# Optimization experiments

Measured on AMD Instinct MI355X. Metric: run time of the kernel, lower is better.

The kernel has to match this reference:

```python
import jax, jax.numpy as jnp
import numpy as np

N, S, D = 8, 448, 768
VS, DS = 50000, 256
VP, DP = 200, 128
VM, DM = 400, 128
VA, DA = 360, 128
EPS_LS = 0.1
LN_EPS = 1e-12
SQRT2 = 1.4142135623730951


def setup_inputs() -> dict:
    key = jax.random.key(0)
    ks = jax.random.split(key, 20)
    total = N * S
    # all sequence lengths == S; next-token prediction uses tokens [0, S-2] as
    # inputs (hidden_sel) and tokens [1, S-1] as targets (target_sel)
    hidden_sel = np.concatenate([i * S + np.arange(S - 1) for i in range(N)]).astype(np.int32)
    target_sel = np.concatenate([i * S + np.arange(1, S) for i in range(N)]).astype(np.int32)
    tokens_lengths = (np.arange(total) % 4).astype(np.int32)  # per-token affix counts
    affix_sel = np.nonzero(tokens_lengths[target_sel] > 0)[0].astype(np.int32)

    def p(k, shape):
        return jax.random.normal(k, shape, jnp.float32) * 0.02

    inp = {
        "tr_hidden_state": jax.random.normal(ks[0], (S, N, D), jnp.float32),
        "affixes_prob": jax.random.uniform(ks[1], (total, VA), dtype=jnp.float32),
        "stems": jax.random.randint(ks[2], (total,), 0, VS, jnp.int32),
        "pos_tags": jax.random.randint(ks[3], (total,), 0, VP, jnp.int32),
        "lm_morphs": jax.random.randint(ks[4], (total,), 0, VM, jnp.int32),
        "hidden_sel_idx": jnp.asarray(hidden_sel),
        "target_sel_idx": jnp.asarray(target_sel),
        "affix_sel_idx": jnp.asarray(affix_sel),
        # stem head
        "stem_emb": p(ks[5], (VS, DS)), "stem_W": p(ks[6], (D, DS)),
        "stem_b": jnp.zeros((DS,)), "stem_g": jnp.ones((DS,)),
        "stem_beta": jnp.zeros((DS,)), "stem_bias": jnp.zeros((VS,)),
        # pos-tag head
        "pos_emb": p(ks[7], (VP, DP)), "pos_W": p(ks[8], (D, DP)),
        "pos_b": jnp.zeros((DP,)), "pos_g": jnp.ones((DP,)),
        "pos_beta": jnp.zeros((DP,)), "pos_bias": jnp.zeros((VP,)),
        # lm-morph head
        "morph_emb": p(ks[9], (VM, DM)), "morph_W": p(ks[10], (D, DM)),
        "morph_b": jnp.zeros((DM,)), "morph_g": jnp.ones((DM,)),
        "morph_beta": jnp.zeros((DM,)), "morph_bias": jnp.zeros((VM,)),
        # affixes head
        "aff_emb": p(ks[11], (VA, DA)), "aff_W": p(ks[12], (D, DA)),
        "aff_b": jnp.zeros((DA,)), "aff_g": jnp.ones((DA,)),
        "aff_beta": jnp.zeros((DA,)), "aff_bias": jnp.zeros((VA,)),
    }
    return inp


def _gelu(x):
    return x * 0.5 * (1.0 + jax.lax.erf(x / SQRT2))


def _ln(x, g, b):
    m = x.mean(-1, keepdims=True)
    v = ((x - m) ** 2).mean(-1, keepdims=True)
    return (x - m) * jax.lax.rsqrt(v + LN_EPS) * g + b


def _head(x, W, b, g, beta, emb, bias):
    h = _ln(_gelu(x @ W + b), g, beta)  # BaseHeadTransform
    return h @ emb.T + bias             # tied decoder + bias


def _ls_nll(lprobs, tgt):
    # label_smoothed_nll_loss with reduce=True, no ignore_index
    nll = -jnp.take_along_axis(lprobs, tgt[:, None], axis=1)[:, 0]
    smooth = -lprobs.sum(-1)
    nll_m, sm_m = nll.mean(), smooth.mean()
    eps_i = EPS_LS / (lprobs.shape[-1] - 1)
    return (1.0 - EPS_LS - eps_i) * nll_m + eps_i * sm_m, nll_m


def reference(tr_hidden_state, affixes_prob, stems, pos_tags, lm_morphs,
              hidden_sel_idx, target_sel_idx, affix_sel_idx,
              stem_emb, stem_W, stem_b, stem_g, stem_beta, stem_bias,
              pos_emb, pos_W, pos_b, pos_g, pos_beta, pos_bias,
              morph_emb, morph_W, morph_b, morph_g, morph_beta, morph_bias,
              aff_emb, aff_W, aff_b, aff_g, aff_beta, aff_bias):
    flat = jnp.transpose(tr_hidden_state, (1, 0, 2)).reshape(N * S, D)
    x = flat[hidden_sel_idx]  # [T, D] ragged gather of predictor states

    stem_lp = jax.nn.log_softmax(_head(x, stem_W, stem_b, stem_g, stem_beta, stem_emb, stem_bias), axis=-1)
    stem_loss, stem_nll = _ls_nll(stem_lp, stems[target_sel_idx])

    pos_lp = jax.nn.log_softmax(_head(x, pos_W, pos_b, pos_g, pos_beta, pos_emb, pos_bias), axis=-1)
    pos_loss, pos_nll = _ls_nll(pos_lp, pos_tags[target_sel_idx])

    morph_lp = jax.nn.log_softmax(_head(x, morph_W, morph_b, morph_g, morph_beta, morph_emb, morph_bias), axis=-1)
    morph_loss, morph_nll = _ls_nll(morph_lp, lm_morphs[target_sel_idx])

    xa = x[affix_sel_idx]                                # tokens with affixes
    ta = affixes_prob[target_sel_idx][affix_sel_idx]     # [Ta, VA]
    z = _head(xa, aff_W, aff_b, aff_g, aff_beta, aff_emb, aff_bias)
    aff_loss = jnp.mean(jnp.maximum(z, 0.0) - z * ta + jnp.log1p(jnp.exp(-jnp.abs(z))))

    return jnp.stack([stem_loss, pos_loss, morph_loss, aff_loss, stem_nll, pos_nll, morph_nll])
```

## Files before the change

kernel.cpp:

```cpp
#include <hip/hip_runtime.h>
#include <cstdint>
#include <cstddef>


typedef __attribute__((ext_vector_type(8))) __bf16 bf16x8;
typedef __attribute__((ext_vector_type(4))) float f32x4;
typedef __attribute__((ext_vector_type(4))) unsigned short u16x4;
typedef __attribute__((ext_vector_type(2))) unsigned short u16x2;

namespace {
constexpr int S_LEN   = 448;
constexpr int N_SEQ   = 8;
constexpr int D_MODEL = 768;
constexpr int TPAD    = 3584;
constexpr int VS = 50000, VP = 200, VM = 400, VA = 360;
constexpr int DS_STEM = 256, DS_POS = 128, DS_MORPH = 128, DS_AFF = 128;
constexpr int VS_PAD = 50176;
constexpr int VCHUNK = 32;
constexpr int VITERS = 3136 / VCHUNK;
constexpr int PERIODS = VITERS / 2;
constexpr float PAD_E = (float)(VS_PAD - VS);
constexpr int NVB_P = 1;
constexpr int NVB_M = 2;
constexpr float LOG2E = 1.4426950408889634f;
constexpr float LN2   = 0.6931471805599453f;
constexpr int B_STEM = 448;
constexpr int B_P    = B_STEM + 112;
constexpr int B_M    = B_P + 224;
constexpr int PREP_G = TPAD * D_MODEL / 256;
constexpr int PREP_T = PREP_G + 491520 / 256;
constexpr int PREP_C = PREP_T + 12753;
}

__device__ __forceinline__ unsigned short f2bf(float f) {
  unsigned int u = __float_as_uint(f);
  unsigned int r = (u + 0x7FFFu + ((u >> 16) & 1u)) >> 16;
  return (unsigned short)r;
}
__device__ __forceinline__ float bf2f(unsigned short u) {
  return __uint_as_float(((unsigned int)u) << 16);
}
__device__ __forceinline__ float fexp2(float x) {
#if __has_builtin(__builtin_amdgcn_exp2f)
  return __builtin_amdgcn_exp2f(x);
#else
  return exp2f(x);
#endif
}

__global__ __launch_bounds__(256) void prep_kernel(
    const float* __restrict__ tr, const int* __restrict__ hsel,
    const int* __restrict__ tsel, const int* __restrict__ asel,
    const int* __restrict__ stems, const int* __restrict__ postags,
    const int* __restrict__ morphs,
    unsigned short* __restrict__ x, int* __restrict__ tgtS, int* __restrict__ tgtP,
    int* __restrict__ tgtM, int* __restrict__ arow, int T, int Ta,
    const float* __restrict__ sW, const float* __restrict__ pW,
    const float* __restrict__ mW, const float* __restrict__ aW,
    unsigned short* __restrict__ wtS, unsigned short* __restrict__ wtP,
    unsigned short* __restrict__ wtM, unsigned short* __restrict__ wtA,
    const float* __restrict__ sE, const float* __restrict__ pE,
    const float* __restrict__ mE, const float* __restrict__ aE,
    const float* __restrict__ sb,
    unsigned short* __restrict__ dS, unsigned short* __restrict__ dP,
    unsigned short* __restrict__ dM, unsigned short* __restrict__ dA,
    float* __restrict__ bp) {
  const int bid = blockIdx.x;
  if (bid < PREP_G) {
    const size_t e = (size_t)bid * 256 + threadIdx.x;
    const int t = (int)(e / D_MODEL);
    const int d = (int)(e % D_MODEL);
    float v = 0.f;
    if (t < T) {
      int idx = hsel[t];
      int n = idx / S_LEN, s = idx % S_LEN;
      v = tr[((size_t)s * N_SEQ + n) * D_MODEL + d];
    }
    x[e] = f2bf(v);
    if (e < (size_t)T) {
      int tt = tsel[e];
      tgtS[e] = stems[tt]; tgtP[e] = postags[tt]; tgtM[e] = morphs[tt];
    }
    if (e < (size_t)Ta) arow[e] = tsel[asel[e]];
  } else if (bid < PREP_T) {
    const int e = (bid - PREP_G) * 256 + threadIdx.x;
    const float* W; unsigned short* Wt; int DS; int local;
    if (e < 196608)      { W = sW; Wt = wtS; DS = 256; local = e; }
    else if (e < 294912) { W = pW; Wt = wtP; DS = 128; local = e - 196608; }
    else if (e < 393216) { W = mW; Wt = wtM; DS = 128; local = e - 294912; }
    else                 { W = aW; Wt = wtA; DS = 128; local = e - 393216; }
    const int n = local / D_MODEL, k = local % D_MODEL;
    Wt[local] = f2bf(W[(size_t)k * DS + n]);
  } else {
    const size_t q = ((size_t)(bid - PREP_T) * 256 + threadIdx.x) * 4;
    if (q >= 13008896) {
      const size_t local = q - 13008896;
      float4 v = make_float4(0.f, 0.f, 0.f, 0.f);
      if (local < (size_t)VS) v = *(const float4*)(sb + local);
      v.x *= LOG2E; v.y *= LOG2E; v.z *= LOG2E; v.w *= LOG2E;
      *(float4*)(bp + local) = v;
      return;
    }
    const float* src; unsigned short* dst; size_t local, real;
    float sc = 1.f;
    if (q < 12845056)      { src = sE; dst = dS; local = q;            real = 12800000; sc = LOG2E; }
    else if (q < 12877824) { src = pE; dst = dP; local = q - 12845056; real = 25600; }
    else if (q < 12943360) { src = mE; dst = dM; local = q - 12877824; real = 51200; }
    else                   { src = aE; dst = dA; local = q - 12943360; real = 46080; }
    float4 v = make_float4(0.f, 0.f, 0.f, 0.f);
    if (local < real) v = *(const float4*)(src + local);
    u16x4 o = { f2bf(v.x * sc), f2bf(v.y * sc), f2bf(v.z * sc), f2bf(v.w * sc) };
    *(u16x4*)(dst + local) = o;
  }
}

template <int NT>
__device__ __forceinline__ void head_body(
    const unsigned short* __restrict__ x, const unsigned short* __restrict__ Wt,
    const float* __restrict__ bvec, const float* __restrict__ gvec,
    const float* __restrict__ betav, unsigned short* __restrict__ hout) {
  constexpr int DS = NT * 16;
  const int lane = threadIdx.x & 63;
  const int wave = threadIdx.x >> 6;
  const int row0 = blockIdx.x * 32 + wave * 16;
  const int lrow = lane & 15;
  const int lk8  = (lane >> 4) * 8;

  f32x4 acc[NT];
#pragma unroll
  for (int nt = 0; nt < NT; ++nt) acc[nt] = f32x4{0.f, 0.f, 0.f, 0.f};

  const unsigned short* xrow = x + (size_t)(row0 + lrow) * D_MODEL + lk8;
#pragma unroll
  for (int ks = 0; ks < 24; ++ks) {
    bf16x8 a = *(const bf16x8*)(xrow + ks * 32);
#pragma unroll
    for (int nt = 0; nt < NT; ++nt) {
      bf16x8 b = *(const bf16x8*)(Wt + (size_t)(nt * 16 + lrow) * D_MODEL + ks * 32 + lk8);
      acc[nt] = __builtin_amdgcn_mfma_f32_16x16x32_bf16(a, b, acc[nt], 0, 0, 0);
    }
  }

  float bb[NT], gg[NT], be[NT];
#pragma unroll
  for (int nt = 0; nt < NT; ++nt) {
    int c = nt * 16 + lrow;
    bb[nt] = bvec[c]; gg[nt] = gvec[c]; be[nt] = betav[c];
  }
#pragma unroll
  for (int r = 0; r < 4; ++r) {
    const int row = row0 + (lane >> 4) * 4 + r;
    float vals[NT];
    float s = 0.f, s2 = 0.f;
#pragma unroll
    for (int nt = 0; nt < NT; ++nt) {
      float v = acc[nt][r] + bb[nt];
      v = 0.5f * v * (1.f + erff(v * 0.70710678118654752f));
      vals[nt] = v; s += v; s2 += v * v;
    }
    s  += __shfl_xor(s, 1);  s  += __shfl_xor(s, 2);  s  += __shfl_xor(s, 4);  s  += __shfl_xor(s, 8);
    s2 += __shfl_xor(s2, 1); s2 += __shfl_xor(s2, 2); s2 += __shfl_xor(s2, 4); s2 += __shfl_xor(s2, 8);
    const float mean = s * (1.f / DS);
    const float var  = s2 * (1.f / DS) - mean * mean;
    const float rstd = rsqrtf(var + 1e-12f);
#pragma unroll
    for (int nt = 0; nt < NT; ++nt) {
      float o = (vals[nt] - mean) * rstd * gg[nt] + be[nt];
      hout[(size_t)row * DS + nt * 16 + lrow] = f2bf(o);
    }
  }
}

__global__ __launch_bounds__(128, 2) void head_all_kernel(
    const unsigned short* __restrict__ x,
    const unsigned short* __restrict__ wtS, const float* __restrict__ sb,
    const float* __restrict__ sg, const float* __restrict__ sbe, unsigned short* __restrict__ hS,
    const unsigned short* __restrict__ wtP, const float* __restrict__ pb,
    const float* __restrict__ pg, const float* __restrict__ pbe, unsigned short* __restrict__ hP,
    const unsigned short* __restrict__ wtM, const float* __restrict__ mb,
    const float* __restrict__ mg, const float* __restrict__ mbe, unsigned short* __restrict__ hM,
    const unsigned short* __restrict__ wtA, const float* __restrict__ ab,
    const float* __restrict__ ag, const float* __restrict__ abe, unsigned short* __restrict__ hA) {
  if (blockIdx.y == 3)      head_body<16>(x, wtS, sb, sg, sbe, hS);
  else if (blockIdx.y == 0) head_body<8>(x, wtP, pb, pg, pbe, hP);
  else if (blockIdx.y == 1) head_body<8>(x, wtM, mb, mg, mbe, hM);
  else                      head_body<8>(x, wtA, ab, ag, abe, hA);
}


__device__ __forceinline__ void stem_role(
    const unsigned short* __restrict__ h, const unsigned short* __restrict__ emb,
    const float* __restrict__ bpad, float* __restrict__ psum,
    float* __restrict__ psum2, char* smem) {
  float* lbias = (float*)(smem + 49152);

  const int f    = blockIdx.x;
  const int xcd  = f & 7;
  const int m    = f >> 3;
  const int bx   = m % 14;
  const int by   = (m / 14) * 8 + xcd;
  const int tid  = threadIdx.x;
  const int lane = tid & 63;
  const int wave = tid >> 6;
  const int lrow = lane & 15;
  const int hi   = lane >> 4;
  const int lk8  = hi * 8;
  const int tok0 = bx * 256 + wave * 64;
  const int vbase0 = by * (VITERS * 16);

  for (int i = tid; i < VITERS * 16; i += 256) lbias[i] = bpad[vbase0 + i];

  bf16x8 hB[4][8];
#pragma unroll
  for (int tt = 0; tt < 4; ++tt)
#pragma unroll
    for (int ks = 0; ks < 8; ++ks)
      hB[tt][ks] = *(const bf16x8*)(h + (size_t)(tok0 + tt * 16 + lrow) * 256 + ks * 32 + lk8);

  const int d0 = tid * 16;
  const int s0 = d0 ^ (((d0 >> 9) & 7) << 4);
  const char* gsA = (const char*)emb + (size_t)vbase0 * 512 + s0;
  const char* gsB = gsA + 4096;

  auto stage_tile = [&](int buf, int tile) {
    __builtin_amdgcn_global_load_lds(
        (const __attribute__((address_space(1))) unsigned int*)(gsA + (size_t)tile * 8192),
        (__attribute__((address_space(3))) unsigned int*)(smem + buf * 8192 + wave * 1024),
        16, 0, 0);
    __builtin_amdgcn_global_load_lds(
        (const __attribute__((address_space(1))) unsigned int*)(gsB + (size_t)tile * 8192),
        (__attribute__((address_space(3))) unsigned int*)(smem + buf * 8192 + 4096 + wave * 1024),
        16, 0, 0);
  };

  int loff[8];
#pragma unroll
  for (int ks = 0; ks < 8; ++ks)
    loff[ks] = (lrow * 512 + ks * 64 + hi * 16) ^ ((lrow & 7) << 4);

  float esum[4] = {0.f, 0.f, 0.f, 0.f};
  float ssum[4] = {0.f, 0.f, 0.f, 0.f};

  stage_tile(0, 0); stage_tile(1, 1);
  stage_tile(2, 2); stage_tile(3, 3);
  __syncthreads();

#pragma unroll 1
  for (int p = 0; p < PERIODS; ++p) {
    if (p < PERIODS - 1) asm volatile("s_waitcnt vmcnt(4)" ::: "memory");
    else                 asm volatile("s_waitcnt vmcnt(0)" ::: "memory");
    __builtin_amdgcn_s_barrier();

    const int t0 = 2 * p, t1 = 2 * p + 1;
    const int b0 = (p % 3) * 2, b1 = b0 + 1;
    const float4 bv0 = *(const float4*)(lbias + t0 * 16 + hi * 4);
    const float4 bv1 = *(const float4*)(lbias + t1 * 16 + hi * 4);

    const char* lp0 = smem + b0 * 8192;
    bf16x8 aA[8];
#pragma unroll
    for (int ks = 0; ks < 8; ++ks)
      aA[ks] = *(const bf16x8*)(lp0 + loff[ks]);

#pragma unroll
    for (int tt = 0; tt < 4; ++tt) {
      f32x4 acc = f32x4{bv0.x, bv0.y, bv0.z, bv0.w};
#pragma unroll
      for (int ks = 0; ks < 8; ++ks)
        acc = __builtin_amdgcn_mfma_f32_16x16x32_bf16(aA[ks], hB[tt][ks], acc, 0, 0, 0);
      esum[tt] += (fexp2(acc[0]) + fexp2(acc[1])) + (fexp2(acc[2]) + fexp2(acc[3]));
      ssum[tt] += (acc[0] + acc[1]) + (acc[2] + acc[3]);
    }

    const char* lp1 = smem + b1 * 8192;
    bf16x8 aB[8];
#pragma unroll
    for (int ks = 0; ks < 8; ++ks)
      aB[ks] = *(const bf16x8*)(lp1 + loff[ks]);

    if (p + 2 < PERIODS) {
      const int nb = ((p + 2) % 3) * 2;
      stage_tile(nb,     2 * (p + 2));
      stage_tile(nb + 1, 2 * (p + 2) + 1);
    }

#pragma unroll
    for (int tt = 0; tt < 4; ++tt) {
      f32x4 acc = f32x4{bv1.x, bv1.y, bv1.z, bv1.w};
#pragma unroll
      for (int ks = 0; ks < 8; ++ks)
        acc = __builtin_amdgcn_mfma_f32_16x16x32_bf16(aB[ks], hB[tt][ks], acc, 0, 0, 0);
      esum[tt] += (fexp2(acc[0]) + fexp2(acc[1])) + (fexp2(acc[2]) + fexp2(acc[3]));
      ssum[tt] += (acc[0] + acc[1]) + (acc[2] + acc[3]);
    }
  }

#pragma unroll
  for (int tt = 0; tt < 4; ++tt) {
    float e = esum[tt], s = ssum[tt];
    e += __shfl_xor(e, 16); e += __shfl_xor(e, 32);
    s += __shfl_xor(s, 16); s += __shfl_xor(s, 32);
    if (hi == 0) {
      const int tok = tok0 + tt * 16 + lrow;
      psum [(size_t)tok * VCHUNK + by] = e;
      psum2[(size_t)tok * VCHUNK + by] = s * LN2;
    }
  }
}

__device__ __forceinline__ void pm_role(
    const unsigned short* __restrict__ h, const unsigned short* __restrict__ emb,
    const float* __restrict__ bias, float* __restrict__ psum,
    float* __restrict__ psum2, int V, int NVB, int vbx, int vby, char* smem) {
  const int tid = threadIdx.x;
  const int lane = tid & 63;
  const int wave4 = tid >> 6;
  const int colbase = vby * 256 + wave4 * 64;
  const int row0 = vbx * 32;
  const int lrow = lane & 15;
  const int hi   = lane >> 4;
  const int lk8  = hi * 8;
  float (*lds_e)[32] = (float(*)[32])smem;
  float (*lds_s)[32] = (float(*)[32])(smem + 512);

  bf16x8 bfr[4][4];
  float bv[4];
  bool mk[4];
#pragma unroll
  for (int nt = 0; nt < 4; ++nt) {
    int col = colbase + nt * 16 + lrow;
#pragma unroll
    for (int ks = 0; ks < 4; ++ks)
      bfr[ks][nt] = *(const bf16x8*)(emb + (size_t)col * 128 + ks * 32 + lk8);
    mk[nt] = (col < V);
    bv[nt] = mk[nt] ? bias[col] : 0.f;
  }

  f32x4 acc[2][4];
#pragma unroll
  for (int rt = 0; rt < 2; ++rt)
#pragma unroll
    for (int nt = 0; nt < 4; ++nt) acc[rt][nt] = f32x4{0.f, 0.f, 0.f, 0.f};

  const unsigned short* hrow = h + (size_t)(row0 + lrow) * 128 + lk8;
#pragma unroll
  for (int ks = 0; ks < 4; ++ks) {
#pragma unroll
    for (int rt = 0; rt < 2; ++rt) {
      bf16x8 a = *(const bf16x8*)(hrow + (size_t)rt * 16 * 128 + ks * 32);
#pragma unroll
      for (int nt = 0; nt < 4; ++nt)
        acc[rt][nt] = __builtin_amdgcn_mfma_f32_16x16x32_bf16(a, bfr[ks][nt], acc[rt][nt], 0, 0, 0);
    }
  }

#pragma unroll
  for (int rt = 0; rt < 2; ++rt)
#pragma unroll
    for (int r = 0; r < 4; ++r) {
      float e = 0.f, s = 0.f;
#pragma unroll
      for (int nt = 0; nt < 4; ++nt) {
        float v = acc[rt][nt][r] + bv[nt];
        float ev = __expf(v);
        e += mk[nt] ? ev : 0.f;
        s += mk[nt] ? v : 0.f;
      }
      e += __shfl_xor(e, 1); e += __shfl_xor(e, 2); e += __shfl_xor(e, 4); e += __shfl_xor(e, 8);
      s += __shfl_xor(s, 1); s += __shfl_xor(s, 2); s += __shfl_xor(s, 4); s += __shfl_xor(s, 8);
      if (lrow == 0) {
        lds_e[wave4][rt * 16 + hi * 4 + r] = e;
        lds_s[wave4][rt * 16 + hi * 4 + r] = s;
      }
    }
  __syncthreads();
  if (tid < 32) {
    const int rr = tid;
    float e = lds_e[0][rr] + lds_e[1][rr] + lds_e[2][rr] + lds_e[3][rr];
    float s = lds_s[0][rr] + lds_s[1][rr] + lds_s[2][rr] + lds_s[3][rr];
    const int row = row0 + rr;
    psum [(size_t)row * NVB + vby] = e;
    psum2[(size_t)row * NVB + vby] = s;
  }
}

__device__ __forceinline__ void aff_role(
    const unsigned short* __restrict__ h, const unsigned short* __restrict__ emb,
    const float* __restrict__ bias, const int* __restrict__ asel,
    const int* __restrict__ arow, const float* __restrict__ aprob,
    float* __restrict__ partial, int Ta, int gaff, int bx, int grp, char* smem) {
  const int tid = threadIdx.x;
  const int lane = tid & 63;
  const int wave4 = tid >> 6;
  const int colbase = grp * 256 + wave4 * 64;
  const int lrow = lane & 15;
  const int lk8  = (lane >> 4) * 8;
  float* wred = (float*)smem;

  bf16x8 bfr[4][4];
  float bv[4];
  bool mk[4];
#pragma unroll
  for (int nt = 0; nt < 4; ++nt) {
    int col = colbase + nt * 16 + lrow;
#pragma unroll
    for (int ks = 0; ks < 4; ++ks)
      bfr[ks][nt] = *(const bf16x8*)(emb + (size_t)col * DS_AFF + ks * 32 + lk8);
    mk[nt] = (col < VA);
    bv[nt] = mk[nt] ? bias[col] : 0.f;
  }

  float lsum = 0.f;
  {
    const int rb = bx * 16;
    const int ia = rb + lrow;
    const int srow = (ia < Ta) ? asel[ia] : 0;
    f32x4 acc[4];
#pragma unroll
    for (int nt = 0; nt < 4; ++nt) acc[nt] = f32x4{0.f, 0.f, 0.f, 0.f};
    const unsigned short* hrow = h + (size_t)srow * DS_AFF + lk8;
#pragma unroll
    for (int ks = 0; ks < 4; ++ks) {
      bf16x8 a = *(const bf16x8*)(hrow + ks * 32);
#pragma unroll
      for (int nt = 0; nt < 4; ++nt)
        acc[nt] = __builtin_amdgcn_mfma_f32_16x16x32_bf16(a, bfr[ks][nt], acc[nt], 0, 0, 0);
    }
#pragma unroll
    for (int r = 0; r < 4; ++r) {
      const int i2 = rb + (lane >> 4) * 4 + r;
      const bool live = (i2 < Ta);
      const int trow = live ? arow[i2] : 0;
#pragma unroll
      for (int nt = 0; nt < 4; ++nt) {
        if (live && mk[nt]) {
          float z = acc[nt][r] + bv[nt];
          float ta = aprob[(size_t)trow * VA + (colbase + nt * 16 + lrow)];
          lsum += fmaxf(z, 0.f) - z * ta + log1pf(__expf(-fabsf(z)));
        }
      }
    }
  }
#pragma unroll
  for (int m = 1; m < 64; m <<= 1) lsum += __shfl_xor(lsum, m);
  if (lane == 0) wred[wave4] = lsum;
  __syncthreads();
  if (tid == 0)
    partial[grp * gaff + bx] = wred[0] + wred[1] + wred[2] + wred[3];
}

__device__ __forceinline__ void tgt_role(
    const unsigned short* __restrict__ hS, const unsigned short* __restrict__ embS,
    const float* __restrict__ bS, const int* __restrict__ tgtS_,
    const unsigned short* __restrict__ hP, const unsigned short* __restrict__ embP,
    const float* __restrict__ bP, const int* __restrict__ tgtP_,
    const unsigned short* __restrict__ hM, const unsigned short* __restrict__ embM,
    const float* __restrict__ bM, const int* __restrict__ tgtM_,
    float* __restrict__ tlog, int T, int vb) {
  const int lane = threadIdx.x & 63;
  const int wave = threadIdx.x >> 6;
  const int t = vb * 4 + wave;
  if (t >= T) return;
  const int tg = tgtS_[t], tp = tgtP_[t], tm = tgtM_[t];
  u16x4 hv = *(const u16x4*)(hS + (size_t)t * 256 + lane * 4);
  u16x4 ev = *(const u16x4*)(embS + (size_t)tg * 256 + lane * 4);
  float d0 = bf2f(hv[0]) * bf2f(ev[0]) + bf2f(hv[1]) * bf2f(ev[1]) +
             bf2f(hv[2]) * bf2f(ev[2]) + bf2f(hv[3]) * bf2f(ev[3]);
  u16x2 hp = *(const u16x2*)(hP + (size_t)t * 128 + lane * 2);
  u16x2 ep = *(const u16x2*)(embP + (size_t)tp * 128 + lane * 2);
  float d1 = bf2f(hp[0]) * bf2f(ep[0]) + bf2f(hp[1]) * bf2f(ep[1]);
  u16x2 hm = *(const u16x2*)(hM + (size_t)t * 128 + lane * 2);
  u16x2 em = *(const u16x2*)(embM + (size_t)tm * 128 + lane * 2);
  float d2 = bf2f(hm[0]) * bf2f(em[0]) + bf2f(hm[1]) * bf2f(em[1]);
#pragma unroll
  for (int m = 1; m < 64; m <<= 1) {
    d0 += __shfl_xor(d0, m); d1 += __shfl_xor(d1, m); d2 += __shfl_xor(d2, m);
  }
  if (lane == 0) {
    tlog[t]            = d0 * LN2 + bS[tg];
    tlog[TPAD + t]     = d1 + bP[tp];
    tlog[2 * TPAD + t] = d2 + bM[tm];
  }
}

__global__ __launch_bounds__(256, 2) void mega_stats_kernel(
    const unsigned short* __restrict__ hS, const unsigned short* __restrict__ embS,
    const float* __restrict__ bpadS, float* __restrict__ psS, float* __restrict__ ps2S,
    const unsigned short* __restrict__ hP, const unsigned short* __restrict__ embP,
    const float* __restrict__ p_bias, float* __restrict__ psP, float* __restrict__ ps2P,
    const unsigned short* __restrict__ hM, const unsigned short* __restrict__ embM,
    const float* __restrict__ m_bias, float* __restrict__ psM, float* __restrict__ ps2M,
    const unsigned short* __restrict__ hA, const unsigned short* __restrict__ embA,
    const float* __restrict__ a_bias, const int* __restrict__ asel,
    const int* __restrict__ arow, const float* __restrict__ aprob,
    float* __restrict__ affp,
    const float* __restrict__ s_bias, const int* __restrict__ tgtS,
    const int* __restrict__ tgtP, const int* __restrict__ tgtM,
    float* __restrict__ tlog, int T, int Ta, int gaff) {
  __shared__ alignas(16) char smem_[55424];
  const int bid = blockIdx.x;
  if (bid < B_STEM) {
    stem_role(hS, embS, bpadS, psS, ps2S, smem_);
  } else if (bid < B_P) {
    pm_role(hP, embP, p_bias, psP, ps2P, VP, NVB_P, bid - B_STEM, 0, smem_);
  } else if (bid < B_M) {
    const int b = bid - B_P;
    pm_role(hM, embM, m_bias, psM, ps2M, VM, NVB_M, b >> 1, b & 1, smem_);
  } else if (bid < B_M + 2 * gaff) {
    const int b = bid - B_M;
    aff_role(hA, embA, a_bias, asel, arow, aprob, affp, Ta, gaff, b >> 1, b & 1, smem_);
  } else {
    tgt_role(hS, embS, s_bias, tgtS, hP, embP, p_bias, tgtP,
             hM, embM, m_bias, tgtM, tlog, T, bid - B_M - 2 * gaff);
  }
}

__global__ __launch_bounds__(256) void combine2_kernel(
    const float* __restrict__ psS, const float* __restrict__ ps2S,
    const float* __restrict__ psP, const float* __restrict__ ps2P,
    const float* __restrict__ psM, const float* __restrict__ ps2M,
    const float* __restrict__ tlog,
    float* __restrict__ nll, float* __restrict__ sm, int T) {
  const int lane = threadIdx.x & 63;
  const int wave = threadIdx.x >> 6;
  const int t = blockIdx.x * 4 + wave;
  if (t >= T) return;

  float z = 0.f, s = 0.f;
  if (lane < VCHUNK) {
    z = psS[(size_t)t * VCHUNK + lane];
    s = ps2S[(size_t)t * VCHUNK + lane];
  }
#pragma unroll
  for (int m = 1; m < 64; m <<= 1) { z += __shfl_xor(z, m); s += __shfl_xor(s, m); }
  if (lane == 0) {
    z -= PAD_E;
    float lz = logf(z);
    nll[t] = lz - tlog[t];
    sm[t]  = (float)VS * lz - s;

    float zP = psP[t], sP = ps2P[t];
    float lzP = logf(zP);
    nll[TPAD + t] = lzP - tlog[TPAD + t];
    sm[TPAD + t]  = (float)VP * lzP - sP;

    float zM = psM[2 * t] + psM[2 * t + 1];
    float sM = ps2M[2 * t] + ps2M[2 * t + 1];
    float lzM = logf(zM);
    nll[2 * TPAD + t] = lzM - tlog[2 * TPAD + t];
    sm[2 * TPAD + t]  = (float)VM * lzM - sM;
  }
}

__global__ __launch_bounds__(256) void finalize_kernel(
    const float* __restrict__ nll, const float* __restrict__ sm,
    const float* __restrict__ affp, int naff, float* __restrict__ out, int T, int Ta) {
  __shared__ float red[256];
  const int tid = threadIdx.x;
  float nll_m[3], sm_m[3];
  for (int h2 = 0; h2 < 3; ++h2) {
    float a = 0.f, b = 0.f;
    for (int t = tid; t < T; t += 256) { a += nll[h2 * TPAD + t]; b += sm[h2 * TPAD + t]; }
    red[tid] = a; __syncthreads();
    for (int s = 128; s > 0; s >>= 1) { if (tid < s) red[tid] += red[tid + s]; __syncthreads(); }
    float asum = red[0]; __syncthreads();
    red[tid] = b; __syncthreads();
    for (int s = 128; s > 0; s >>= 1) { if (tid < s) red[tid] += red[tid + s]; __syncthreads(); }
    float bsm = red[0]; __syncthreads();
    nll_m[h2] = asum / (float)T;
    sm_m[h2]  = bsm / (float)T;
  }
  float av = 0.f;
  for (int i = tid; i < naff; i += 256) av += affp[i];
  red[tid] = av; __syncthreads();
  for (int s = 128; s > 0; s >>= 1) { if (tid < s) red[tid] += red[tid + s]; __syncthreads(); }
  if (tid == 0) {
    const float Vv[3] = {(float)VS, (float)VP, (float)VM};
    for (int h2 = 0; h2 < 3; ++h2) {
      float eps_i = 0.1f / (Vv[h2] - 1.f);
      out[h2] = (1.0f - 0.1f - eps_i) * nll_m[h2] + eps_i * sm_m[h2];
      out[4 + h2] = nll_m[h2];
    }
    out[3] = red[0] / ((float)Ta * (float)VA);
  }
}

extern "C" void kernel_launch(void* const* d_in, const int* in_sizes, int n_in,
                              void* d_out, int out_size, void* d_ws, size_t ws_size,
                              hipStream_t stream) {
  const float* tr      = (const float*)d_in[0];
  const float* aprob   = (const float*)d_in[1];
  const int* stems     = (const int*)d_in[2];
  const int* postags   = (const int*)d_in[3];
  const int* morphs    = (const int*)d_in[4];
  const int* hsel      = (const int*)d_in[5];
  const int* tsel      = (const int*)d_in[6];
  const int* asel      = (const int*)d_in[7];
  const float* s_emb = (const float*)d_in[8],  *s_W = (const float*)d_in[9];
  const float* s_b   = (const float*)d_in[10], *s_g = (const float*)d_in[11];
  const float* s_be  = (const float*)d_in[12], *s_bias = (const float*)d_in[13];
  const float* p_emb = (const float*)d_in[14], *p_W = (const float*)d_in[15];
  const float* p_b   = (const float*)d_in[16], *p_g = (const float*)d_in[17];
  const float* p_be  = (const float*)d_in[18], *p_bias = (const float*)d_in[19];
  const float* m_emb = (const float*)d_in[20], *m_W = (const float*)d_in[21];
  const float* m_b   = (const float*)d_in[22], *m_g = (const float*)d_in[23];
  const float* m_be  = (const float*)d_in[24], *m_bias = (const float*)d_in[25];
  const float* a_emb = (const float*)d_in[26], *a_W = (const float*)d_in[27];
  const float* a_b   = (const float*)d_in[28], *a_g = (const float*)d_in[29];
  const float* a_be  = (const float*)d_in[30], *a_bias = (const float*)d_in[31];

  const int T  = in_sizes[5];
  const int Ta = in_sizes[7];

  size_t off = 0;
  auto alloc = [&](size_t nbytes) -> char* {
    char* p = (char*)d_ws + off;
    off = (off + nbytes + 255) & ~(size_t)255;
    return p;
  };
  unsigned short* x    = (unsigned short*)alloc((size_t)TPAD * D_MODEL * 2);
  unsigned short* wtS  = (unsigned short*)alloc((size_t)DS_STEM * D_MODEL * 2);
  unsigned short* wtP  = (unsigned short*)alloc((size_t)DS_POS * D_MODEL * 2);
  unsigned short* wtM  = (unsigned short*)alloc((size_t)DS_MORPH * D_MODEL * 2);
  unsigned short* wtA  = (unsigned short*)alloc((size_t)DS_AFF * D_MODEL * 2);
  unsigned short* embS = (unsigned short*)alloc((size_t)VS_PAD * DS_STEM * 2);
  unsigned short* embP = (unsigned short*)alloc((size_t)256 * DS_POS * 2);
  unsigned short* embM = (unsigned short*)alloc((size_t)512 * DS_MORPH * 2);
  unsigned short* embA = (unsigned short*)alloc((size_t)512 * DS_AFF * 2);
  unsigned short* hS   = (unsigned short*)alloc((size_t)TPAD * DS_STEM * 2);
  unsigned short* hP   = (unsigned short*)alloc((size_t)TPAD * DS_POS * 2);
  unsigned short* hM   = (unsigned short*)alloc((size_t)TPAD * DS_MORPH * 2);
  unsigned short* hA   = (unsigned short*)alloc((size_t)TPAD * DS_AFF * 2);
  float* bpadS = (float*)alloc((size_t)VS_PAD * 4);
  float* psS   = (float*)alloc((size_t)TPAD * VCHUNK * 4);
  float* ps2S  = (float*)alloc((size_t)TPAD * VCHUNK * 4);
  float* psP   = (float*)alloc((size_t)TPAD * NVB_P * 4);
  float* ps2P  = (float*)alloc((size_t)TPAD * NVB_P * 4);
  float* psM   = (float*)alloc((size_t)TPAD * NVB_M * 4);
  float* ps2M  = (float*)alloc((size_t)TPAD * NVB_M * 4);
  float* tlog  = (float*)alloc((size_t)3 * TPAD * 4);
  int*   tgtS  = (int*)alloc((size_t)TPAD * 4);
  int*   tgtP  = (int*)alloc((size_t)TPAD * 4);
  int*   tgtM  = (int*)alloc((size_t)TPAD * 4);
  int*   arow  = (int*)alloc((size_t)TPAD * 4);
  float* nllb  = (float*)alloc((size_t)3 * TPAD * 4);
  float* smb   = (float*)alloc((size_t)3 * TPAD * 4);
  float* affp  = (float*)alloc(2048);
  (void)ws_size; (void)n_in; (void)out_size;

  const int gaff = (Ta + 15) / 16;
  const int tgtb = (T + 3) / 4;

  prep_kernel<<<PREP_C, 256, 0, stream>>>(
      tr, hsel, tsel, asel, stems, postags, morphs, x, tgtS, tgtP, tgtM, arow, T, Ta,
      s_W, p_W, m_W, a_W, wtS, wtP, wtM, wtA,
      s_emb, p_emb, m_emb, a_emb, s_bias, embS, embP, embM, embA, bpadS);
  head_all_kernel<<<dim3(TPAD / 32, 4), 128, 0, stream>>>(
      x, wtS, s_b, s_g, s_be, hS, wtP, p_b, p_g, p_be, hP,
      wtM, m_b, m_g, m_be, hM, wtA, a_b, a_g, a_be, hA);
  mega_stats_kernel<<<B_M + 2 * gaff + tgtb, 256, 0, stream>>>(
      hS, embS, bpadS, psS, ps2S,
      hP, embP, p_bias, psP, ps2P,
      hM, embM, m_bias, psM, ps2M,
      hA, embA, a_bias, asel, arow, aprob, affp,
      s_bias, tgtS, tgtP, tgtM, tlog, T, Ta, gaff);
  combine2_kernel<<<(T + 3) / 4, 256, 0, stream>>>(psS, ps2S, psP, ps2P, psM, ps2M, tlog, nllb, smb, T);
  finalize_kernel<<<1, 256, 0, stream>>>(nllb, smb, affp, gaff * 2, (float*)d_out, T, Ta);
}
```

Measured before the change: 226.1 us.

## Tile weight transposes through LDS and widen head blocks to four waves

The weight-transpose section of the prep kernel now uses 64x64 LDS tiles, so both global reads and bf16 writes are coalesced, replacing the strided per-element gather. It drops from 1920 blocks to 120. Separately, the head kernel goes from 128 to 256 threads per block, covering 64 rows per block so each block has four waves and half as many blocks. The transpose tile adds 16.6KB of static shared memory to every prep block, including the gather and embedding-conversion roles that do not use it, which could limit occupancy there.

```diff
diff --git a/kernel.cpp b/kernel.cpp
--- a/kernel.cpp
+++ b/kernel.cpp
@@ -28,7 +28,7 @@
 constexpr int B_P    = B_STEM + 112;
 constexpr int B_M    = B_P + 224;
 constexpr int PREP_G = TPAD * D_MODEL / 256;
-constexpr int PREP_T = PREP_G + 491520 / 256;
+constexpr int PREP_T = PREP_G + 120;
 constexpr int PREP_C = PREP_T + 12753;
 }
 
@@ -65,9 +65,11 @@
     unsigned short* __restrict__ dS, unsigned short* __restrict__ dP,
     unsigned short* __restrict__ dM, unsigned short* __restrict__ dA,
     float* __restrict__ bp) {
+  __shared__ float tile[64][65];
   const int bid = blockIdx.x;
+  const int tid = threadIdx.x;
   if (bid < PREP_G) {
-    const size_t e = (size_t)bid * 256 + threadIdx.x;
+    const size_t e = (size_t)bid * 256 + tid;
     const int t = (int)(e / D_MODEL);
     const int d = (int)(e % D_MODEL);
     float v = 0.f;
@@ -83,16 +85,26 @@
     }
     if (e < (size_t)Ta) arow[e] = tsel[asel[e]];
   } else if (bid < PREP_T) {
-    const int e = (bid - PREP_G) * 256 + threadIdx.x;
-    const float* W; unsigned short* Wt; int DS; int local;
-    if (e < 196608)      { W = sW; Wt = wtS; DS = 256; local = e; }
-    else if (e < 294912) { W = pW; Wt = wtP; DS = 128; local = e - 196608; }
-    else if (e < 393216) { W = mW; Wt = wtM; DS = 128; local = e - 294912; }
-    else                 { W = aW; Wt = wtA; DS = 128; local = e - 393216; }
-    const int n = local / D_MODEL, k = local % D_MODEL;
-    Wt[local] = f2bf(W[(size_t)k * DS + n]);
+    const int tt = bid - PREP_G;
+    const float* W; unsigned short* Wt; int DS, kt, nt;
+    if (tt < 48) { W = sW; Wt = wtS; DS = 256; kt = tt >> 2; nt = tt & 3; }
+    else {
+      int u = tt - 48; const int h = u / 24; u %= 24;
+      kt = u >> 1; nt = u & 1; DS = 128;
+      W  = (h == 0) ? pW : (h == 1) ? mW : aW;
+      Wt = (h == 0) ? wtP : (h == 1) ? wtM : wtA;
+    }
+    const int k0 = kt * 64, n0 = nt * 64;
+    const int rr = tid >> 6, cc = tid & 63;
+#pragma unroll
+    for (int i = 0; i < 16; ++i)
+      tile[i * 4 + rr][cc] = W[(size_t)(k0 + i * 4 + rr) * DS + n0 + cc];
+    __syncthreads();
+#pragma unroll
+    for (int i = 0; i < 16; ++i)
+      Wt[(size_t)(n0 + i * 4 + rr) * D_MODEL + k0 + cc] = f2bf(tile[cc][i * 4 + rr]);
   } else {
-    const size_t q = ((size_t)(bid - PREP_T) * 256 + threadIdx.x) * 4;
+    const size_t q = ((size_t)(bid - PREP_T) * 256 + tid) * 4;
     if (q >= 13008896) {
       const size_t local = q - 13008896;
       float4 v = make_float4(0.f, 0.f, 0.f, 0.f);
@@ -122,7 +134,7 @@
   constexpr int DS = NT * 16;
   const int lane = threadIdx.x & 63;
   const int wave = threadIdx.x >> 6;
-  const int row0 = blockIdx.x * 32 + wave * 16;
+  const int row0 = blockIdx.x * 64 + wave * 16;
   const int lrow = lane & 15;
   const int lk8  = (lane >> 4) * 8;
 
@@ -171,7 +183,7 @@
   }
 }
 
-__global__ __launch_bounds__(128, 2) void head_all_kernel(
+__global__ __launch_bounds__(256, 2) void head_all_kernel(
     const unsigned short* __restrict__ x,
     const unsigned short* __restrict__ wtS, const float* __restrict__ sb,
     const float* __restrict__ sg, const float* __restrict__ sbe, unsigned short* __restrict__ hS,
@@ -222,13 +234,13 @@
   const char* gsA = (const char*)emb + (size_t)vbase0 * 512 + s0;
   const char* gsB = gsA + 4096;
 
-  auto stage_tile = [&](int buf, int tile) {
+  auto stage_tile = [&](int buf, int tile2) {
     __builtin_amdgcn_global_load_lds(
-        (const __attribute__((address_space(1))) unsigned int*)(gsA + (size_t)tile * 8192),
+        (const __attribute__((address_space(1))) unsigned int*)(gsA + (size_t)tile2 * 8192),
         (__attribute__((address_space(3))) unsigned int*)(smem + buf * 8192 + wave * 1024),
         16, 0, 0);
     __builtin_amdgcn_global_load_lds(
-        (const __attribute__((address_space(1))) unsigned int*)(gsB + (size_t)tile * 8192),
+        (const __attribute__((address_space(1))) unsigned int*)(gsB + (size_t)tile2 * 8192),
         (__attribute__((address_space(3))) unsigned int*)(smem + buf * 8192 + 4096 + wave * 1024),
         16, 0, 0);
   };
@@ -655,7 +667,7 @@
       tr, hsel, tsel, asel, stems, postags, morphs, x, tgtS, tgtP, tgtM, arow, T, Ta,
       s_W, p_W, m_W, a_W, wtS, wtP, wtM, wtA,
       s_emb, p_emb, m_emb, a_emb, s_bias, embS, embP, embM, embA, bpadS);
-  head_all_kernel<<<dim3(TPAD / 32, 4), 128, 0, stream>>>(
+  head_all_kernel<<<dim3(TPAD / 64, 4), 256, 0, stream>>>(
       x, wtS, s_b, s_g, s_be, hS, wtP, p_b, p_g, p_be, hP,
       wtM, m_b, m_g, m_be, hM, wtA, a_b, a_g, a_be, hA);
   mega_stats_kernel<<<B_M + 2 * gaff + tgtb, 256, 0, stream>>>(
```

New measurement: 221.2 us. 2.2% less time.
